# Kernel optimization log

Hardware: AMD Instinct MI355X
Metric: run time of the kernel (lower is better)

The kernel has to match this reference:

```python
import jax, jax.numpy as jnp
import numpy as np

B, S, D = 4, 2048, 1024
H, DH = 16, 64
THETA = 10000.0


def _rope_tables(seq_len, dim):
    # freqs_cis = exp(i * t * f), here as cos/sin tables, shape [S, dim//2]
    freqs = 1.0 / (THETA ** (jnp.arange(0, dim, 2, dtype=jnp.float32) / dim))
    ang = jnp.outer(jnp.arange(seq_len, dtype=jnp.float32), freqs)
    return jnp.cos(ang), jnp.sin(ang)


def _apply_rope(x, cos, sin):
    # x: [B,S,H,DH]; pairs are interleaved (x[...,2i], x[...,2i+1])
    xe = x[..., 0::2]
    xo = x[..., 1::2]
    c = cos[None, :, None, :]
    s = sin[None, :, None, :]
    out = jnp.stack([xe * c - xo * s, xe * s + xo * c], axis=-1)
    return out.reshape(x.shape).astype(x.dtype)


def setup_inputs() -> dict:
    key = jax.random.key(0)
    ks = jax.random.split(key, 5)
    x = jax.random.normal(ks[0], (B, S, D), dtype=jnp.float32)
    Wq = jax.random.normal(ks[1], (D, D), dtype=jnp.float32) * 0.02
    Wk = jax.random.normal(ks[2], (D, D), dtype=jnp.float32) * 0.02
    Wv = jax.random.normal(ks[3], (D, D), dtype=jnp.float32) * 0.02
    Wo = jax.random.normal(ks[4], (D, D), dtype=jnp.float32) * 0.02
    lambdas = jnp.zeros((2,), dtype=jnp.float32)
    return {"x": x, "Wq": Wq, "Wk": Wk, "Wv": Wv, "Wo": Wo, "lambdas": lambdas}


def reference(x, Wq, Wk, Wv, Wo, lambdas):
    scale = 1.0 / np.sqrt(DH)
    q = (x @ Wq.T).reshape(B, S, H, DH)
    k = (x @ Wk.T).reshape(B, S, H, DH)
    v = (x @ Wv.T).reshape(B, S, H, DH)
    cos, sin = _rope_tables(S, DH)
    q = _apply_rope(q, cos, sin)
    k = _apply_rope(k, cos, sin)
    # explicit QK^T with causal mask, softmax, then @V (dropout is identity in eval)
    attn = jnp.einsum('bshd,bthd->bhst', q, k) * scale  # [B,H,S,S]
    causal = jnp.tril(jnp.ones((S, S), dtype=bool))
    attn = jnp.where(causal[None, None], attn, -jnp.inf)
    probs = jax.nn.softmax(attn, axis=-1)
    head_out = jnp.einsum('bhst,bthd->bshd', probs, v)  # [B,S,H,DH]
    out = head_out.reshape(B, S, D) @ Wo.T
    return out
```

## Files before the change

### kernel.cpp

```cpp
#include <hip/hip_runtime.h>
#include <math.h>

static constexpr int Bsz = 4, Sq = 2048, Dm = 1024, NH = 16, DHd = 64;
static constexpr int Mrows = Bsz * Sq;
static constexpr float ROPE_LN = 0.14391156831212787f;

typedef _Float16 half8 __attribute__((ext_vector_type(8)));
typedef _Float16 half4v __attribute__((ext_vector_type(4)));
typedef float f32x4 __attribute__((ext_vector_type(4)));

__device__ __forceinline__ void gl_lds16(const void* g, void* l) {
    __builtin_amdgcn_global_load_lds(
        (const __attribute__((address_space(1))) void*)g,
        (__attribute__((address_space(3))) void*)l, 16, 0, 0);
}

__global__ __launch_bounds__(256) void prep_kernel(
    const float* __restrict__ x,
    const float* __restrict__ Wq, const float* __restrict__ Wk,
    const float* __restrict__ Wv, const float* __restrict__ Wo,
    _Float16* __restrict__ xh,
    _Float16* __restrict__ Wqh, _Float16* __restrict__ Wkh,
    _Float16* __restrict__ Wvh, _Float16* __restrict__ Woh,
    float2* __restrict__ rope)
{
    const int i = blockIdx.x * 256 + threadIdx.x;
    if (i < 2097152) {
        const float4 v = ((const float4*)x)[i];
        half4v hv;
        hv[0] = (_Float16)v.x; hv[1] = (_Float16)v.y;
        hv[2] = (_Float16)v.z; hv[3] = (_Float16)v.w;
        ((half4v*)xh)[i] = hv;
    } else if (i < 3145728) {
        const int w = (i - 2097152) >> 18;
        const int off = (i - 2097152) & 262143;
        const float* s = (w == 0) ? Wq : (w == 1) ? Wk : (w == 2) ? Wv : Wo;
        _Float16* d = (w == 0) ? Wqh : (w == 1) ? Wkh : (w == 2) ? Wvh : Woh;
        const float sc = (w == 0) ? 0.125f : 1.0f;
        const float4 v = ((const float4*)s)[off];
        half4v hv;
        hv[0] = (_Float16)(v.x * sc); hv[1] = (_Float16)(v.y * sc);
        hv[2] = (_Float16)(v.z * sc); hv[3] = (_Float16)(v.w * sc);
        ((half4v*)d)[off] = hv;
    } else {
        const int t = i - 3145728;
        const int pos = t >> 5, j = t & 31;
        const float f = expf(-ROPE_LN * (float)(2 * j));
        const float a = (float)pos * f;
        rope[t] = make_float2(cosf(a), sinf(a));
    }
}

template <typename OutT, int MODE>
__device__ __forceinline__ void mfma_gemm_body(
    const _Float16* __restrict__ A, const _Float16* __restrict__ W,
    OutT* __restrict__ C, const float2* __restrict__ rope, int K, int N,
    int m0, int n0)
{
    __shared__ _Float16 As[2][128 * 32];
    __shared__ _Float16 Bs[2][128 * 32];

    const int tid = threadIdx.x;
    const int wave = tid >> 6, lane = tid & 63;
    const int quad = lane >> 4, l16 = lane & 15;
    const int wm = (wave >> 1) * 64, wn = (wave & 1) * 64;

    const _Float16* gA[2]; const _Float16* gB[2];
    int lOff[2];
    #pragma unroll
    for (int i = 0; i < 2; ++i) {
        const int F = (wave * 2 + i) * 64 + lane;
        const int r = F >> 2, cp = F & 3;
        const int c = cp ^ ((r >> 1) & 3);
        gA[i] = A + (size_t)(m0 + r) * K + c * 8;
        gB[i] = W + (size_t)(n0 + r) * K + c * 8;
        lOff[i] = (wave * 2 + i) * 512;
    }

    const int sw = (l16 >> 1) & 3;
    int offA[4], offB[4];
    #pragma unroll
    for (int t = 0; t < 4; ++t) {
        offA[t] = (wm + t * 16 + l16) * 32 + ((quad ^ sw) * 8);
        offB[t] = (wn + t * 16 + l16) * 32 + ((quad ^ sw) * 8);
    }

    f32x4 acc[4][4];
    #pragma unroll
    for (int im = 0; im < 4; ++im)
        #pragma unroll
        for (int nb = 0; nb < 4; ++nb)
            #pragma unroll
            for (int r = 0; r < 4; ++r) acc[im][nb][r] = 0.f;

    for (int k0 = 0; k0 < K; k0 += 64) {
        __syncthreads();
        #pragma unroll
        for (int kh = 0; kh < 2; ++kh)
            #pragma unroll
            for (int i = 0; i < 2; ++i) {
                gl_lds16(gA[i] + k0 + kh * 32, &As[kh][lOff[i]]);
                gl_lds16(gB[i] + k0 + kh * 32, &Bs[kh][lOff[i]]);
            }
        __syncthreads();

        #pragma unroll
        for (int kh = 0; kh < 2; ++kh) {
            half8 a[4], b[4];
            #pragma unroll
            for (int t = 0; t < 4; ++t) {
                a[t] = *(const half8*)&As[kh][offA[t]];
                b[t] = *(const half8*)&Bs[kh][offB[t]];
            }
            #pragma unroll
            for (int im = 0; im < 4; ++im)
                #pragma unroll
                for (int nb = 0; nb < 4; ++nb)
                    acc[im][nb] = __builtin_amdgcn_mfma_f32_16x16x32_f16(
                        a[im], b[nb], acc[im][nb], 0, 0, 0);
        }
    }

    #pragma unroll
    for (int nb = 0; nb < 4; ++nb) {
        const int n = n0 + wn + nb * 16 + l16;
        if constexpr (MODE == 2) {
            const int hb = ((m0 + wm) >> 11) * 16 + (n >> 6);
            const int dh = n & 63;
            const int tb = (m0 + wm) & (Sq - 1);
            half8 v0, v1;
            #pragma unroll
            for (int r = 0; r < 4; ++r)
                #pragma unroll
                for (int im = 0; im < 4; ++im) {
                    const int idx = r * 4 + im;
                    const _Float16 h = (_Float16)acc[im][nb][r];
                    if (idx < 8) v0[idx] = h; else v1[idx - 8] = h;
                }
            _Float16* dst = C + (((size_t)hb * 64 + dh) << 11) + tb + quad * 16;
            *(half8*)dst = v0;
            *(half8*)(dst + 8) = v1;
        } else {
            const int j = (n & 63) >> 1;
            #pragma unroll
            for (int im = 0; im < 4; ++im) {
                #pragma unroll
                for (int r = 0; r < 4; ++r) {
                    const int m = m0 + wm + im * 16 + quad * 4 + r;
                    float v = acc[im][nb][r];
                    if constexpr (MODE == 1) {
                        const int pos = m & (Sq - 1);
                        const float2 cs = rope[pos * 32 + j];
                        const float vp = __shfl_xor(v, 1);
                        v = (n & 1) ? (vp * cs.y + v * cs.x)
                                    : (v * cs.x - vp * cs.y);
                        C[(size_t)m * N + n] = (_Float16)v;
                    } else {
                        C[(size_t)m * N + n] = v;
                    }
                }
            }
        }
    }
}

__device__ __forceinline__ void xcd_swizzle(int& m0, int& n0) {
    const int orig = blockIdx.x + (blockIdx.y << 3);
    const int xcd = orig & 7, j = orig >> 3;
    m0 = (xcd * 8 + (j >> 3)) * 128;
    n0 = (j & 7) * 128;
}

__global__ __launch_bounds__(256) void qkv_mfma_kernel(
    const _Float16* __restrict__ xh,
    const _Float16* __restrict__ Wq, const _Float16* __restrict__ Wk,
    const _Float16* __restrict__ Wv,
    _Float16* __restrict__ Qo, _Float16* __restrict__ Ko,
    _Float16* __restrict__ VTp, const float2* __restrict__ rope)
{
    int m0, n0;
    xcd_swizzle(m0, n0);
    const int z = blockIdx.z;
    if (z == 0)
        mfma_gemm_body<_Float16, 1>(xh, Wq, Qo, rope, Dm, Dm, m0, n0);
    else if (z == 1)
        mfma_gemm_body<_Float16, 1>(xh, Wk, Ko, rope, Dm, Dm, m0, n0);
    else
        mfma_gemm_body<_Float16, 2>(xh, Wv, VTp, nullptr, Dm, Dm, m0, n0);
}

__global__ __launch_bounds__(256) void oproj_mfma_kernel(
    const _Float16* __restrict__ HOh, const _Float16* __restrict__ Wo,
    float* __restrict__ out)
{
    int m0, n0;
    xcd_swizzle(m0, n0);
    mfma_gemm_body<float, 0>(HOh, Wo, out, nullptr, Dm, Dm, m0, n0);
}

__global__ __launch_bounds__(256) void attn_mfma_kernel(
    const _Float16* __restrict__ Q, const _Float16* __restrict__ K,
    const _Float16* __restrict__ VT, _Float16* __restrict__ HO)
{
    __shared__ _Float16 Ks[2][64 * 64];
    __shared__ _Float16 Vs[2][64 * 64];
    __shared__ _Float16 Ps[4][32][72];

    const int tid = threadIdx.x;
    const int wave = tid >> 6, lane = tid & 63;
    const int quad = lane >> 4, l16 = lane & 15;
    const int id = blockIdx.x;
    const int hb = id & 63;
    const int qi = 15 - (id >> 6);
    const int h = hb & 15, b = hb >> 4;
    const int q0 = qi * 128;
    const size_t base = (size_t)b * Sq * Dm + (size_t)h * DHd;
    const size_t vtbase = (size_t)hb * 64 * Sq;

    half8 ones;
    #pragma unroll
    for (int i = 0; i < 8; ++i) ones[i] = (_Float16)1.0f;

    half8 aQ[2][2];
    #pragma unroll
    for (int mf = 0; mf < 2; ++mf) {
        const _Float16* qrow =
            Q + base + (size_t)(q0 + wave * 32 + mf * 16 + l16) * Dm + quad * 8;
        aQ[mf][0] = *(const half8*)(qrow);
        aQ[mf][1] = *(const half8*)(qrow + 32);
    }

    f32x4 Oacc[2][4];
    #pragma unroll
    for (int mf = 0; mf < 2; ++mf)
        #pragma unroll
        for (int nb = 0; nb < 4; ++nb)
            #pragma unroll
            for (int r = 0; r < 4; ++r) Oacc[mf][nb][r] = 0.f;
    f32x4 lacc[2];
    #pragma unroll
    for (int mf = 0; mf < 2; ++mf)
        #pragma unroll
        for (int r = 0; r < 4; ++r) lacc[mf][r] = 0.f;

    auto stage_tile = [&](int t0, int buf) {
        #pragma unroll
        for (int i = 0; i < 2; ++i) {
            const int F = (wave * 2 + i) * 64 + lane;
            const int r = F >> 3;
            const int cl = (F & 7) ^ (r & 7);
            gl_lds16(K + base + (size_t)(t0 + r) * Dm + cl * 8,
                     &Ks[buf][(wave * 2 + i) * 512]);
            gl_lds16(VT + vtbase + ((size_t)r << 11) + t0 + cl * 8,
                     &Vs[buf][(wave * 2 + i) * 512]);
        }
    };

    auto do_tile = [&](int buf, int dd, bool diag) {
        const _Float16* Kb = Ks[buf];
        const _Float16* Vb = Vs[buf];

        f32x4 sacc[2][4];
        #pragma unroll
        for (int mf = 0; mf < 2; ++mf)
            #pragma unroll
            for (int nb = 0; nb < 4; ++nb)
                #pragma unroll
                for (int r = 0; r < 4; ++r) sacc[mf][nb][r] = 0.f;
        __builtin_amdgcn_s_setprio(1);
        #pragma unroll
        for (int kstep = 0; kstep < 2; ++kstep) {
            #pragma unroll
            for (int nb = 0; nb < 4; ++nb) {
                const int krow = nb * 16 + l16;
                const int kch = (kstep * 4 + quad) ^ (krow & 7);
                const half8 bK = *(const half8*)&Kb[krow * 64 + kch * 8];
                #pragma unroll
                for (int mf = 0; mf < 2; ++mf)
                    sacc[mf][nb] = __builtin_amdgcn_mfma_f32_16x16x32_f16(
                        aQ[mf][kstep], bK, sacc[mf][nb], 0, 0, 0);
            }
        }
        __builtin_amdgcn_s_setprio(0);

        #pragma unroll
        for (int mf = 0; mf < 2; ++mf)
            #pragma unroll
            for (int r = 0; r < 4; ++r) {
                half4v pk;
                #pragma unroll
                for (int nb = 0; nb < 4; ++nb) {
                    float v = sacc[mf][nb][r];
                    if (diag && (nb * 16 + l16 + dd >
                                 wave * 32 + mf * 16 + quad * 4 + r))
                        v = -1.0e4f;
                    pk[nb] = (_Float16)__expf(v);
                }
                *(half4v*)&Ps[wave][mf * 16 + quad * 4 + r][l16 * 4] = pk;
            }

        __builtin_amdgcn_s_setprio(1);
        #pragma unroll
        for (int kstep = 0; kstep < 2; ++kstep) {
            half8 aP[2];
            #pragma unroll
            for (int mf = 0; mf < 2; ++mf) {
                aP[mf] = *(const half8*)
                    &Ps[wave][mf * 16 + l16][kstep * 32 + quad * 8];
                lacc[mf] = __builtin_amdgcn_mfma_f32_16x16x32_f16(
                    aP[mf], ones, lacc[mf], 0, 0, 0);
            }
            #pragma unroll
            for (int nb = 0; nb < 4; ++nb) {
                const int vrow = nb * 16 + l16;
                const int vch = (kstep * 4 + quad) ^ (vrow & 7);
                const half8 bV = *(const half8*)&Vb[vrow * 64 + vch * 8];
                #pragma unroll
                for (int mf = 0; mf < 2; ++mf)
                    Oacc[mf][nb] = __builtin_amdgcn_mfma_f32_16x16x32_f16(
                        aP[mf], bV, Oacc[mf][nb], 0, 0, 0);
            }
        }
        __builtin_amdgcn_s_setprio(0);
    };

    const int nt = 2 * qi + 2;
    stage_tile(0, 0);
    for (int t = 0; t < nt; ++t) {
        __syncthreads();
        if (t + 1 < nt) stage_tile((t + 1) * 64, (t + 1) & 1);
        do_tile(t & 1, t * 64 - q0, t >= nt - 2);
    }

    #pragma unroll
    for (int mf = 0; mf < 2; ++mf) {
        float inv[4];
        #pragma unroll
        for (int r = 0; r < 4; ++r) inv[r] = 1.0f / lacc[mf][r];
        #pragma unroll
        for (int nb = 0; nb < 4; ++nb)
            #pragma unroll
            for (int r = 0; r < 4; ++r) {
                const int row = wave * 32 + mf * 16 + quad * 4 + r;
                HO[base + (size_t)(q0 + row) * Dm + nb * 16 + l16] =
                    (_Float16)(Oacc[mf][nb][r] * inv[r]);
            }
    }
}

extern "C" void kernel_launch(void* const* d_in, const int* in_sizes, int n_in,
                              void* d_out, int out_size, void* d_ws, size_t ws_size,
                              hipStream_t stream)
{
    const float* x  = (const float*)d_in[0];
    const float* Wq = (const float*)d_in[1];
    const float* Wk = (const float*)d_in[2];
    const float* Wv = (const float*)d_in[3];
    const float* Wo = (const float*)d_in[4];
    float* out = (float*)d_out;

    const size_t matX = (size_t)Mrows * Dm;
    const size_t matW = (size_t)Dm * Dm;

    _Float16* xh  = (_Float16*)d_ws;
    _Float16* Wqh = xh + matX;
    _Float16* Wkh = Wqh + matW;
    _Float16* Wvh = Wkh + matW;
    _Float16* Woh = Wvh + matW;
    _Float16* Qh  = Woh + matW;
    _Float16* Kh  = Qh + matX;
    _Float16* VTp = Kh + matX;
    _Float16* HOh = VTp + matX;
    float2* rope  = (float2*)(HOh + matX);

    dim3 blk(256);
    prep_kernel<<<(3145728 + 65536) / 256, blk, 0, stream>>>(
        x, Wq, Wk, Wv, Wo, xh, Wqh, Wkh, Wvh, Woh, rope);
    qkv_mfma_kernel<<<dim3(Dm / 128, Mrows / 128, 3), blk, 0, stream>>>(
        xh, Wqh, Wkh, Wvh, Qh, Kh, VTp, rope);
    attn_mfma_kernel<<<dim3(16 * NH * Bsz), blk, 0, stream>>>(
        Qh, Kh, VTp, HOh);
    oproj_mfma_kernel<<<dim3(Dm / 128, Mrows / 128, 1), blk, 0, stream>>>(
        HOh, Woh, out);
}
```

Baseline: 243.2 us.

## Triple-buffer GEMM LDS tiles with async prefetch two k-steps ahead

Replaces the synchronous load-then-compute loop of the MFMA GEMM body with a three-slot LDS ring buffer. Global-to-LDS loads for step t+2 are issued while step t computes, and the loop waits with a partial vmcnt wait plus one barrier per 32-wide k-step instead of two __syncthreads per 64-wide step. The aim is to hide global memory latency behind the MFMAs, at the cost of 50% more LDS per block, which may lower occupancy. Correctness relies on the hand-written vmcnt count matching the four loads issued per stage, and on the LDS reads from a slot completing before that slot is overwritten.

```diff
diff --git a/kernel.cpp b/kernel.cpp
--- a/kernel.cpp
+++ b/kernel.cpp
@@ -57,8 +57,8 @@
     OutT* __restrict__ C, const float2* __restrict__ rope, int K, int N,
     int m0, int n0)
 {
-    __shared__ _Float16 As[2][128 * 32];
-    __shared__ _Float16 Bs[2][128 * 32];
+    __shared__ _Float16 As[3][128 * 32];
+    __shared__ _Float16 Bs[3][128 * 32];
 
     const int tid = threadIdx.x;
     const int wave = tid >> 6, lane = tid & 63;
@@ -93,32 +93,45 @@
             #pragma unroll
             for (int r = 0; r < 4; ++r) acc[im][nb][r] = 0.f;
 
-    for (int k0 = 0; k0 < K; k0 += 64) {
-        __syncthreads();
-        #pragma unroll
-        for (int kh = 0; kh < 2; ++kh)
-            #pragma unroll
-            for (int i = 0; i < 2; ++i) {
-                gl_lds16(gA[i] + k0 + kh * 32, &As[kh][lOff[i]]);
-                gl_lds16(gB[i] + k0 + kh * 32, &Bs[kh][lOff[i]]);
-            }
-        __syncthreads();
-
-        #pragma unroll
-        for (int kh = 0; kh < 2; ++kh) {
-            half8 a[4], b[4];
-            #pragma unroll
-            for (int t = 0; t < 4; ++t) {
-                a[t] = *(const half8*)&As[kh][offA[t]];
-                b[t] = *(const half8*)&Bs[kh][offB[t]];
-            }
-            #pragma unroll
-            for (int im = 0; im < 4; ++im)
-                #pragma unroll
-                for (int nb = 0; nb < 4; ++nb)
-                    acc[im][nb] = __builtin_amdgcn_mfma_f32_16x16x32_f16(
-                        a[im], b[nb], acc[im][nb], 0, 0, 0);
-        }
+    auto stage = [&](int s, int t) {
+        const int koff = t * 32;
+        #pragma unroll
+        for (int i = 0; i < 2; ++i) {
+            gl_lds16(gA[i] + koff, &As[s][lOff[i]]);
+            gl_lds16(gB[i] + koff, &Bs[s][lOff[i]]);
+        }
+    };
+
+    const int KS = K >> 5;
+    stage(0, 0);
+    stage(1, 1);
+    int slot = 0, ps = 2;
+    for (int t = 0; t < KS; ++t) {
+        if (t < KS - 1)
+            asm volatile("s_waitcnt vmcnt(4)" ::: "memory");
+        else
+            asm volatile("s_waitcnt vmcnt(0)" ::: "memory");
+        __builtin_amdgcn_s_barrier();
+
+        const _Float16* Ab = As[slot];
+        const _Float16* Bb = Bs[slot];
+        half8 a[4], b[4];
+        #pragma unroll
+        for (int q = 0; q < 4; ++q) {
+            a[q] = *(const half8*)&Ab[offA[q]];
+            b[q] = *(const half8*)&Bb[offB[q]];
+        }
+        if (t + 2 < KS) stage(ps, t + 2);
+
+        #pragma unroll
+        for (int im = 0; im < 4; ++im)
+            #pragma unroll
+            for (int nb = 0; nb < 4; ++nb)
+                acc[im][nb] = __builtin_amdgcn_mfma_f32_16x16x32_f16(
+                    a[im], b[nb], acc[im][nb], 0, 0, 0);
+
+        slot = (slot == 2) ? 0 : slot + 1;
+        ps = (ps == 2) ? 0 : ps + 1;
     }
 
     #pragma unroll
```

Result: slower. 283.3 us (+16.5%).
